# Optimization experiments

Measured on AMD Instinct MI355X. Metric: run time of the kernel, lower is better.

Reference implementation:

```python
import jax, jax.numpy as jnp
import numpy as np

B, S, E, H, D, W = 2, 4096, 768, 12, 64, 256  # batch, seq, hidden, heads, head_dim, one-sided window


def setup_inputs() -> dict:
    key = jax.random.key(0)
    ks = jax.random.split(key, 4)
    s = 0.02
    return {
        "hidden_states": jax.random.normal(ks[0], (B, S, E), jnp.float32),
        "Wq": jax.random.normal(ks[1], (E, E), jnp.float32) * s,
        "bq": jnp.zeros((E,), jnp.float32),
        "Wk": jax.random.normal(ks[2], (E, E), jnp.float32) * s,
        "bk": jnp.zeros((E,), jnp.float32),
        "Wv": jax.random.normal(ks[3], (E, E), jnp.float32) * s,
        "bv": jnp.zeros((E,), jnp.float32),
    }


def _band_attention(q, k, v):
    # q,k,v: [B,H,S,D]. Sliding-window attention: query i attends keys j with |j-i| <= W,
    # clipped to [0, S) -- same math as sliding_chunks_matmul_qk + mask_invalid_locations
    # + softmax + sliding_chunks_matmul_pv (dropout p=0, eval mode).
    C = S // W  # number of query chunks of size W

    def ext(x):
        # gather, for each chunk c, the keys of chunks c-1, c, c+1 (zero padded at edges)
        xp = jnp.pad(x, ((0, 0), (0, 0), (W, W), (0, 0)))
        xc = xp.reshape(B, H, C + 2, W, D)
        return jnp.concatenate([xc[:, :, 0:C], xc[:, :, 1:C + 1], xc[:, :, 2:C + 2]], axis=3)  # [B,H,C,3W,D]

    qc = q.reshape(B, H, C, W, D)
    ke = ext(k)
    ve = ext(v)
    scores = jnp.einsum('bhcpd,bhctd->bhcpt', qc, ke)  # [B,H,C,W,3W]

    p = jnp.arange(W)[:, None]            # query offset within chunk
    t = jnp.arange(3 * W)[None, :]        # key offset within extended window
    rel = t - W - p                       # j - i  (relative position)
    j = jnp.arange(C)[:, None, None] * W + (t - W)[None]  # global key index [C,W,3W]
    mask = (jnp.abs(rel)[None] <= W) & (j >= 0) & (j < S)  # band + sequence-boundary mask

    scores = jnp.where(mask[None, None], scores, -1e30)
    probs = jax.nn.softmax(scores, axis=-1)
    out = jnp.einsum('bhcpt,bhctd->bhcpd', probs, ve)
    return out.reshape(B, H, S, D)


def reference(hidden_states, Wq, bq, Wk, bk, Wv, bv):
    scale = 1.0 / float(np.sqrt(D))
    q = (hidden_states @ Wq + bq) * scale  # q scaled by 1/sqrt(head_dim) as in original
    k = hidden_states @ Wk + bk
    v = hidden_states @ Wv + bv
    split = lambda x: x.reshape(B, S, H, D).transpose(0, 2, 1, 3)  # [B,H,S,D]
    out = _band_attention(split(q), split(k), split(v))
    return out.transpose(0, 2, 1, 3).reshape(B, S, E)  # [B,S,E] context_layer
```

## Files before the change

### kernel.cpp

```cpp
#include <hip/hip_runtime.h>

#define BB 2
#define SS 4096
#define EE 768
#define HH 12
#define DD 64
#define WW 256

typedef __attribute__((ext_vector_type(8))) short short8;
typedef __attribute__((ext_vector_type(4))) short short4v;
typedef __attribute__((ext_vector_type(4))) float floatx4;

#define MFMA16(a, b, c) __builtin_amdgcn_mfma_f32_16x16x32_bf16(a, b, c, 0, 0, 0)

__device__ __forceinline__ float bf2f(short x) {
    union { unsigned u; float f; } v;
    v.u = ((unsigned)(unsigned short)x) << 16;
    return v.f;
}

__device__ __forceinline__ short f2bf(float x) {
    union { float f; unsigned u; } v;
    v.f = x;
    unsigned r = v.u + 0x7fffu + ((v.u >> 16) & 1u);
    return (short)(r >> 16);
}

__device__ __forceinline__ int imin(int a, int b) { return a < b ? a : b; }
__device__ __forceinline__ int imax(int a, int b) { return a > b ? a : b; }

__device__ __forceinline__ void gload_lds16(const short* g, short* l) {
    __builtin_amdgcn_global_load_lds(
        (const __attribute__((address_space(1))) unsigned*)g,
        (__attribute__((address_space(3))) unsigned*)l, 16, 0, 0);
}

__global__ __launch_bounds__(256) void prep(
    const float* __restrict__ hidden, const float* __restrict__ W0,
    const float* __restrict__ W1, const float* __restrict__ W2,
    short* __restrict__ Xb, short* __restrict__ Wt) {
    __shared__ short t[32][33];
    int bid = blockIdx.x;
    int tid = threadIdx.x;
    if (bid < 6144) {
        size_t i4 = (size_t)bid * 256 + tid;
        floatx4 f = *(const floatx4*)(hidden + i4 * 4);
        short4v s;
#pragma unroll
        for (int k = 0; k < 4; k++) s[k] = f2bf(f[k]);
        *(short4v*)(Xb + i4 * 4) = s;
    } else {
        int tmp = bid - 6144;
        int z = tmp / 576, r = tmp % 576;
        int bx = r % 24, by = r / 24;
        const float* in = (z == 0) ? W0 : (z == 1) ? W1 : W2;
        short* op = Wt + (size_t)z * EE * EE;
        int y0 = by * 32;
        int ty = tid >> 3, tx4 = tid & 7;
        floatx4 f = *(const floatx4*)&in[(size_t)(y0 + ty) * EE + bx * 32 + tx4 * 4];
#pragma unroll
        for (int k = 0; k < 4; k++) t[ty][tx4 * 4 + k] = f2bf(f[k]);
        __syncthreads();
        int A = tid >> 3, B0 = (tid & 7) * 4;
        short4v v;
#pragma unroll
        for (int k = 0; k < 4; k++) v[k] = t[B0 + k][A];
        *(short4v*)&op[(size_t)(bx * 32 + A) * EE + y0 + B0] = v;
    }
}

__global__ __launch_bounds__(256, 4) void qkv_gemm(
    const short* __restrict__ Xb, const short* __restrict__ Wt,
    const float* __restrict__ Bq, const float* __restrict__ Bk, const float* __restrict__ Bv,
    short* __restrict__ Qo, short* __restrict__ Ko, short* __restrict__ Vto) {
    int z = blockIdx.z;
    const short* Wz = Wt + (size_t)z * EE * EE;
    const float* bias = (z == 0) ? Bq : (z == 1) ? Bk : Bv;

    __shared__ __align__(16) short As[3][64 * 32];
    __shared__ __align__(16) short Bs[3][128 * 32];
    int tid = threadIdx.x;
    int m0 = blockIdx.x * 64, n0 = blockIdx.y * 128;
    int wave = tid >> 6, lane = tid & 63, lquad = lane >> 4, lrow = lane & 15;
    int wm = (wave & 1) * 32, wn = (wave >> 1) * 64;

    floatx4 acc[2][4] = {};

    int ca = tid;
    int ua = (ca & 7) ^ ((ca >> 3) & 7);
    int ras = (ca >> 3) * 2 + (ua >> 2), qas = (ua & 3) * 8;
    int cb1 = 256 + tid;
    int ub1 = (cb1 & 7) ^ ((cb1 >> 3) & 7);
    int rb1 = (cb1 >> 3) * 2 + (ub1 >> 2), qb1 = (ub1 & 3) * 8;

    const short* xa = &Xb[(size_t)(m0 + ras) * EE + qas];
    const short* wa0 = &Wz[(size_t)(n0 + ras) * EE + qas];
    const short* wa1 = &Wz[(size_t)(n0 + rb1) * EE + qb1];

    auto issueTile = [&](int t) {
        int k0 = t * 32;
        int bs = t % 3;
        gload_lds16(xa + k0, &As[bs][ca * 8]);
        gload_lds16(wa0 + k0, &Bs[bs][ca * 8]);
        gload_lds16(wa1 + k0, &Bs[bs][cb1 * 8]);
    };

    int offA[2], offB[4];
#pragma unroll
    for (int mt = 0; mt < 2; mt++) {
        int ra = wm + mt * 16 + lrow;
        int sa = (lquad | ((ra & 1) << 2)) ^ ((ra >> 1) & 7);
        offA[mt] = (ra >> 1) * 64 + sa * 8;
    }
#pragma unroll
    for (int nt = 0; nt < 4; nt++) {
        int rb = wn + nt * 16 + lrow;
        int sb = (lquad | ((rb & 1) << 2)) ^ ((rb >> 1) & 7);
        offB[nt] = (rb >> 1) * 64 + sb * 8;
    }

    issueTile(0);
    issueTile(1);

#pragma unroll
    for (int t = 0; t < 24; ++t) {
        if (t < 23) asm volatile("s_waitcnt vmcnt(3)" ::: "memory");
        else        asm volatile("s_waitcnt vmcnt(0)" ::: "memory");
        __builtin_amdgcn_sched_barrier(0);
        __builtin_amdgcn_s_barrier();
        asm volatile("" ::: "memory");

        if (t + 2 < 24) issueTile(t + 2);

        int bs = t % 3;
        short8 af[2], bfv[4];
#pragma unroll
        for (int mt = 0; mt < 2; mt++)
            af[mt] = *(short8*)&As[bs][offA[mt]];
#pragma unroll
        for (int nt = 0; nt < 4; nt++)
            bfv[nt] = *(short8*)&Bs[bs][offB[nt]];
#pragma unroll
        for (int mt = 0; mt < 2; mt++)
#pragma unroll
            for (int nt = 0; nt < 4; nt++)
                acc[mt][nt] = MFMA16(af[mt], bfv[nt], acc[mt][nt]);
    }

    if (z == 2) {
        for (int nt = 0; nt < 4; nt++) {
            int gn = n0 + wn + nt * 16 + lrow;
            float bv = bias[gn];
            int h = gn >> 6, d = gn & 63;
            for (int mt = 0; mt < 2; mt++) {
                int gm0 = m0 + wm + mt * 16 + lquad * 4;
                int b = gm0 >> 12, s = gm0 & (SS - 1);
                short4v pk;
                for (int r = 0; r < 4; r++) pk[r] = f2bf(acc[mt][nt][r] + bv);
                *(short4v*)&Vto[(((size_t)(b * HH + h)) * DD + d) * SS + s] = pk;
            }
        }
    } else {
        short* out = (z == 0) ? Qo : Ko;
        float scale = (z == 0) ? 0.125f : 1.0f;
        for (int nt = 0; nt < 4; nt++) {
            int gn = n0 + wn + nt * 16 + lrow;
            float bv = bias[gn];
            int h = gn >> 6, d = gn & 63;
            for (int mt = 0; mt < 2; mt++) {
                int gmb = m0 + wm + mt * 16 + lquad * 4;
                for (int r = 0; r < 4; r++) {
                    int gm = gmb + r;
                    int b = gm >> 12, s = gm & (SS - 1);
                    float v = (acc[mt][nt][r] + bv) * scale;
                    out[(((size_t)(b * HH + h)) * SS + s) * DD + d] = f2bf(v);
                }
            }
        }
    }
}

__global__ __launch_bounds__(256) void band_attn(
    const short* __restrict__ Q, const short* __restrict__ K,
    const short* __restrict__ Vt, float* __restrict__ out) {
    int hb = blockIdx.x;
    int h = hb % HH, b = hb / HH;
    int chunk = blockIdx.y;
    int tid = threadIdx.x;
    int wave = tid >> 6, lane = tid & 63, lquad = lane >> 4, lrow = lane & 15;
    int qbase = chunk * 128 + wave * 32;

    const short* Qh = Q + ((size_t)(b * HH + h)) * SS * DD;
    const short* Kh = K + ((size_t)(b * HH + h)) * SS * DD;
    const short* Vh = Vt + ((size_t)(b * HH + h)) * DD * SS;

    __shared__ __align__(16) short Ks[2][64 * 72];
    __shared__ __align__(16) short Vs[2][64 * 72];
    __shared__ __align__(16) short Ps[4][16 * 72];
    short* Pw = &Ps[wave][0];

    short8 qf[2][2];
#pragma unroll
    for (int m = 0; m < 2; m++)
#pragma unroll
        for (int hh = 0; hh < 2; hh++)
            qf[m][hh] = *(const short8*)&Qh[(size_t)(qbase + m * 16 + lrow) * DD + hh * 32 + lquad * 8];

    floatx4 o[2][4] = {};
    float ls[2] = {0.0f, 0.0f};

    int kwin = chunk * 128 - WW;
    int srow = tid >> 3;
    int scol = (tid & 7) * 8;
    int tlo = wave >> 1;

    short8 kreg[2], vreg[2];
    auto loadTile = [&](int t) {
        int ks0 = kwin + t * 64;
#pragma unroll
        for (int i = 0; i < 2; i++) {
            int r = srow + i * 32;
            int gk = imin(imax(ks0 + r, 0), SS - 1);
            kreg[i] = *(const short8*)&Kh[(size_t)gk * DD + scol];
            int gv = imin(imax(ks0 + scol, 0), SS - 8);
            vreg[i] = *(const short8*)&Vh[(size_t)r * SS + gv];
        }
    };
    auto storeTile = [&](int buf) {
#pragma unroll
        for (int i = 0; i < 2; i++) {
            int r = srow + i * 32;
            *(short8*)&Ks[buf][r * 72 + scol] = kreg[i];
            *(short8*)&Vs[buf][r * 72 + scol] = vreg[i];
        }
    };

    loadTile(0);
    storeTile(0);
    __syncthreads();

    for (int t = 0; t < 10; t++) {
        int buf = t & 1;
        if (t < 9) loadTile(t + 1);

        if ((unsigned)(t - tlo) < 9u) {
            int ks0 = kwin + t * 64;
            short8 kf[4][2], vf[4][2];
#pragma unroll
            for (int kt = 0; kt < 4; kt++)
#pragma unroll
                for (int hh = 0; hh < 2; hh++)
                    kf[kt][hh] = *(short8*)&Ks[buf][(kt * 16 + lrow) * 72 + hh * 32 + lquad * 8];
#pragma unroll
            for (int nt = 0; nt < 4; nt++)
#pragma unroll
                for (int hh = 0; hh < 2; hh++)
                    vf[nt][hh] = *(short8*)&Vs[buf][(nt * 16 + lrow) * 72 + hh * 32 + lquad * 8];

            int d0 = ks0 - qbase;
            bool interior = (d0 >= -225) && (d0 <= 193) && (ks0 >= 0) && (ks0 <= SS - 64);

            __builtin_amdgcn_s_setprio(1);
#pragma unroll
            for (int m = 0; m < 2; m++) {
                int q = qbase + m * 16 + lrow;
                floatx4 s[4];
#pragma unroll
                for (int kt = 0; kt < 4; kt++) {
                    floatx4 zz = {};
                    s[kt] = MFMA16(kf[kt][0], qf[m][0], zz);
                    s[kt] = MFMA16(kf[kt][1], qf[m][1], s[kt]);
                }
                float lacc = 0.0f;
                if (interior) {
#pragma unroll
                    for (int kt = 0; kt < 4; kt++) {
                        short4v pk;
#pragma unroll
                        for (int r = 0; r < 4; r++) {
                            float p = __expf(s[kt][r]);
                            pk[r] = f2bf(p);
                            lacc += bf2f(pk[r]);
                        }
                        *(short4v*)&Pw[lrow * 72 + kt * 16 + lquad * 4] = pk;
                    }
                } else {
#pragma unroll
                    for (int kt = 0; kt < 4; kt++) {
                        short4v pk;
#pragma unroll
                        for (int r = 0; r < 4; r++) {
                            int key = ks0 + kt * 16 + lquad * 4 + r;
                            bool valid = ((unsigned)(key - q + WW) <= 2u * WW) && ((unsigned)key < SS);
                            float p = valid ? __expf(s[kt][r]) : 0.0f;
                            pk[r] = f2bf(p);
                            lacc += bf2f(pk[r]);
                        }
                        *(short4v*)&Pw[lrow * 72 + kt * 16 + lquad * 4] = pk;
                    }
                }
                ls[m] += lacc;
                asm volatile("" ::: "memory");
                short8 ap0 = *(short8*)&Pw[lrow * 72 + lquad * 8];
                short8 ap1 = *(short8*)&Pw[lrow * 72 + 32 + lquad * 8];
#pragma unroll
                for (int nt = 0; nt < 4; nt++) {
                    o[m][nt] = MFMA16(ap0, vf[nt][0], o[m][nt]);
                    o[m][nt] = MFMA16(ap1, vf[nt][1], o[m][nt]);
                }
            }
            __builtin_amdgcn_s_setprio(0);
        }

        if (t < 9) storeTile(buf ^ 1);
        __syncthreads();
    }

#pragma unroll
    for (int m = 0; m < 2; m++) {
        ls[m] += __shfl_xor(ls[m], 16, 64);
        ls[m] += __shfl_xor(ls[m], 32, 64);
        ls[m] = 1.0f / ls[m];
    }

#pragma unroll
    for (int m = 0; m < 2; m++) {
#pragma unroll
        for (int r = 0; r < 4; r++) {
            float linv = __shfl(ls[m], lquad * 4 + r, 64);
            int s = qbase + m * 16 + lquad * 4 + r;
#pragma unroll
            for (int nt = 0; nt < 4; nt++)
                out[((size_t)b * SS + s) * EE + h * DD + nt * 16 + lrow] = o[m][nt][r] * linv;
        }
    }
}

extern "C" void kernel_launch(void* const* d_in, const int* in_sizes, int n_in,
                              void* d_out, int out_size, void* d_ws, size_t ws_size,
                              hipStream_t stream) {
    const float* hidden = (const float*)d_in[0];
    const float* Wq = (const float*)d_in[1];
    const float* bq = (const float*)d_in[2];
    const float* Wk = (const float*)d_in[3];
    const float* bk = (const float*)d_in[4];
    const float* Wv = (const float*)d_in[5];
    const float* bv = (const float*)d_in[6];
    float* out = (float*)d_out;

    short* ws = (short*)d_ws;
    const size_t WSZ = (size_t)EE * EE;
    const size_t QSZ = (size_t)BB * HH * SS * DD;
    short* Wt = ws;
    short* Qb = Wt + 3 * WSZ;
    short* Kb = Qb + QSZ;
    short* Vtb = Kb + QSZ;
    short* Xb = (short*)d_out;

    prep<<<dim3(6144 + 3 * 576, 1, 1), 256, 0, stream>>>(hidden, Wq, Wk, Wv, Xb, Wt);

    qkv_gemm<<<dim3(128, 6, 3), 256, 0, stream>>>(Xb, Wt, bq, bk, bv, Qb, Kb, Vtb);

    band_attn<<<dim3(HH * BB, SS / 128, 1), 256, 0, stream>>>(Qb, Kb, Vtb, out);
}
```

Baseline: 184.5 us.

## Fuse fp32-to-bf16 conversion of hidden states into the QKV GEMM A-tile load

The separate prep pass that converted hidden states to bf16 is removed. The GEMM now loads fp32 activations into registers, converts them, and writes them to LDS, double-buffered across iterations, while B tiles still stream directly into LDS. This saves a full write and re-read of the bf16 activation copy. In exchange it reads twice the bytes for A, and every z-slice and n-block converts the same rows again. It also adds register pressure and an extra LDS wait and barrier per iteration.

```diff
diff --git a/kernel.cpp b/kernel.cpp
--- a/kernel.cpp
+++ b/kernel.cpp
@@ -36,41 +36,30 @@
 }
 
 __global__ __launch_bounds__(256) void prep(
-    const float* __restrict__ hidden, const float* __restrict__ W0,
-    const float* __restrict__ W1, const float* __restrict__ W2,
-    short* __restrict__ Xb, short* __restrict__ Wt) {
+    const float* __restrict__ W0, const float* __restrict__ W1,
+    const float* __restrict__ W2, short* __restrict__ Wt) {
     __shared__ short t[32][33];
     int bid = blockIdx.x;
     int tid = threadIdx.x;
-    if (bid < 6144) {
-        size_t i4 = (size_t)bid * 256 + tid;
-        floatx4 f = *(const floatx4*)(hidden + i4 * 4);
-        short4v s;
-#pragma unroll
-        for (int k = 0; k < 4; k++) s[k] = f2bf(f[k]);
-        *(short4v*)(Xb + i4 * 4) = s;
-    } else {
-        int tmp = bid - 6144;
-        int z = tmp / 576, r = tmp % 576;
-        int bx = r % 24, by = r / 24;
-        const float* in = (z == 0) ? W0 : (z == 1) ? W1 : W2;
-        short* op = Wt + (size_t)z * EE * EE;
-        int y0 = by * 32;
-        int ty = tid >> 3, tx4 = tid & 7;
-        floatx4 f = *(const floatx4*)&in[(size_t)(y0 + ty) * EE + bx * 32 + tx4 * 4];
-#pragma unroll
-        for (int k = 0; k < 4; k++) t[ty][tx4 * 4 + k] = f2bf(f[k]);
-        __syncthreads();
-        int A = tid >> 3, B0 = (tid & 7) * 4;
-        short4v v;
-#pragma unroll
-        for (int k = 0; k < 4; k++) v[k] = t[B0 + k][A];
-        *(short4v*)&op[(size_t)(bx * 32 + A) * EE + y0 + B0] = v;
-    }
+    int z = bid / 576, r = bid % 576;
+    int bx = r % 24, by = r / 24;
+    const float* in = (z == 0) ? W0 : (z == 1) ? W1 : W2;
+    short* op = Wt + (size_t)z * EE * EE;
+    int y0 = by * 32;
+    int ty = tid >> 3, tx4 = tid & 7;
+    floatx4 f = *(const floatx4*)&in[(size_t)(y0 + ty) * EE + bx * 32 + tx4 * 4];
+#pragma unroll
+    for (int k = 0; k < 4; k++) t[ty][tx4 * 4 + k] = f2bf(f[k]);
+    __syncthreads();
+    int A = tid >> 3, B0 = (tid & 7) * 4;
+    short4v v;
+#pragma unroll
+    for (int k = 0; k < 4; k++) v[k] = t[B0 + k][A];
+    *(short4v*)&op[(size_t)(bx * 32 + A) * EE + y0 + B0] = v;
 }
 
 __global__ __launch_bounds__(256, 4) void qkv_gemm(
-    const short* __restrict__ Xb, const short* __restrict__ Wt,
+    const float* __restrict__ X, const short* __restrict__ Wt,
     const float* __restrict__ Bq, const float* __restrict__ Bk, const float* __restrict__ Bv,
     short* __restrict__ Qo, short* __restrict__ Ko, short* __restrict__ Vto) {
     int z = blockIdx.z;
@@ -92,25 +81,30 @@
     int cb1 = 256 + tid;
     int ub1 = (cb1 & 7) ^ ((cb1 >> 3) & 7);
     int rb1 = (cb1 >> 3) * 2 + (ub1 >> 2), qb1 = (ub1 & 3) * 8;
-
-    const short* xa = &Xb[(size_t)(m0 + ras) * EE + qas];
     const short* wa0 = &Wz[(size_t)(n0 + ras) * EE + qas];
     const short* wa1 = &Wz[(size_t)(n0 + rb1) * EE + qb1];
 
-    auto issueTile = [&](int t) {
-        int k0 = t * 32;
-        int bs = t % 3;
-        gload_lds16(xa + k0, &As[bs][ca * 8]);
+    int ra = tid >> 2, qa = tid & 3;
+    int cA = (ra >> 1) * 8 + ((qa | ((ra & 1) << 2)) ^ ((ra >> 1) & 7));
+    const float* xsrc = &X[(size_t)(m0 + ra) * EE + qa * 8];
+
+    auto issueB = [&](int t) {
+        int k0 = t * 32, bs = t % 3;
         gload_lds16(wa0 + k0, &Bs[bs][ca * 8]);
         gload_lds16(wa1 + k0, &Bs[bs][cb1 * 8]);
     };
 
+#define ISSUE_A(r0, r1, t) { const floatx4* p = (const floatx4*)(xsrc + (t) * 32); r0 = p[0]; r1 = p[1]; }
+#define WRITE_A(r0, r1, t) { short8 s8_; \
+    _Pragma("unroll") for (int j_ = 0; j_ < 4; j_++) { s8_[j_] = f2bf(r0[j_]); s8_[j_ + 4] = f2bf(r1[j_]); } \
+    *(short8*)&As[(t) % 3][cA * 8] = s8_; }
+
     int offA[2], offB[4];
 #pragma unroll
     for (int mt = 0; mt < 2; mt++) {
-        int ra = wm + mt * 16 + lrow;
-        int sa = (lquad | ((ra & 1) << 2)) ^ ((ra >> 1) & 7);
-        offA[mt] = (ra >> 1) * 64 + sa * 8;
+        int rr = wm + mt * 16 + lrow;
+        int sa = (lquad | ((rr & 1) << 2)) ^ ((rr >> 1) & 7);
+        offA[mt] = (rr >> 1) * 64 + sa * 8;
     }
 #pragma unroll
     for (int nt = 0; nt < 4; nt++) {
@@ -119,32 +113,47 @@
         offB[nt] = (rb >> 1) * 64 + sb * 8;
     }
 
-    issueTile(0);
-    issueTile(1);
+    floatx4 a0A, a1A, a0B, a1B;
+
+    issueB(0); ISSUE_A(a0A, a1A, 0);
+    issueB(1); ISSUE_A(a0B, a1B, 1);
+    asm volatile("s_waitcnt vmcnt(4)" ::: "memory");
+    WRITE_A(a0A, a1A, 0);
+    asm volatile("s_waitcnt lgkmcnt(0)" ::: "memory");
+    __builtin_amdgcn_s_barrier();
+    asm volatile("" ::: "memory");
 
 #pragma unroll
     for (int t = 0; t < 24; ++t) {
-        if (t < 23) asm volatile("s_waitcnt vmcnt(3)" ::: "memory");
-        else        asm volatile("s_waitcnt vmcnt(0)" ::: "memory");
+        if (t + 2 < 24) {
+            issueB(t + 2);
+            if (t & 1) { ISSUE_A(a0B, a1B, t + 2); } else { ISSUE_A(a0A, a1A, t + 2); }
+        }
+
+        int bs = t % 3;
+        short8 af[2], bfv[4];
+#pragma unroll
+        for (int mt = 0; mt < 2; mt++)
+            af[mt] = *(short8*)&As[bs][offA[mt]];
+#pragma unroll
+        for (int nt = 0; nt < 4; nt++)
+            bfv[nt] = *(short8*)&Bs[bs][offB[nt]];
+#pragma unroll
+        for (int mt = 0; mt < 2; mt++)
+#pragma unroll
+            for (int nt = 0; nt < 4; nt++)
+                acc[mt][nt] = MFMA16(af[mt], bfv[nt], acc[mt][nt]);
+
+        if (t + 1 < 24) {
+            if (t + 2 < 24) asm volatile("s_waitcnt vmcnt(4)" ::: "memory");
+            else            asm volatile("s_waitcnt vmcnt(0)" ::: "memory");
+            if (t & 1) { WRITE_A(a0A, a1A, t + 1); } else { WRITE_A(a0B, a1B, t + 1); }
+        }
+
         __builtin_amdgcn_sched_barrier(0);
+        asm volatile("s_waitcnt lgkmcnt(0)" ::: "memory");
         __builtin_amdgcn_s_barrier();
         asm volatile("" ::: "memory");
-
-        if (t + 2 < 24) issueTile(t + 2);
-
-        int bs = t % 3;
-        short8 af[2], bfv[4];
-#pragma unroll
-        for (int mt = 0; mt < 2; mt++)
-            af[mt] = *(short8*)&As[bs][offA[mt]];
-#pragma unroll
-        for (int nt = 0; nt < 4; nt++)
-            bfv[nt] = *(short8*)&Bs[bs][offB[nt]];
-#pragma unroll
-        for (int mt = 0; mt < 2; mt++)
-#pragma unroll
-            for (int nt = 0; nt < 4; nt++)
-                acc[mt][nt] = MFMA16(af[mt], bfv[nt], acc[mt][nt]);
     }
 
     if (z == 2) {
@@ -178,6 +187,8 @@
             }
         }
     }
+#undef ISSUE_A
+#undef WRITE_A
 }
 
 __global__ __launch_bounds__(256) void band_attn(
@@ -355,11 +366,10 @@
     short* Qb = Wt + 3 * WSZ;
     short* Kb = Qb + QSZ;
     short* Vtb = Kb + QSZ;
-    short* Xb = (short*)d_out;
-
-    prep<<<dim3(6144 + 3 * 576, 1, 1), 256, 0, stream>>>(hidden, Wq, Wk, Wv, Xb, Wt);
-
-    qkv_gemm<<<dim3(128, 6, 3), 256, 0, stream>>>(Xb, Wt, bq, bk, bv, Qb, Kb, Vtb);
+
+    prep<<<dim3(3 * 576, 1, 1), 256, 0, stream>>>(Wq, Wk, Wv, Wt);
+
+    qkv_gemm<<<dim3(128, 6, 3), 256, 0, stream>>>(hidden, Wt, bq, bk, bv, Qb, Kb, Vtb);
 
     band_attn<<<dim3(HH * BB, SS / 128, 1), 256, 0, stream>>>(Qb, Kb, Vtb, out);
 }
```

After: 182.4 us. No clear change (-1.1%).

## Replace LDS-staged pipelined QKV GEMM with direct global-to-register fragment loads

Applied to the files above, without the earlier changes.

The QKV projection GEMM drops its triple-buffered LDS staging (global_load_lds with swizzled layout, waitcnt and barriers). Each wave now loads its MFMA A and B fragments straight from global memory into registers inside a fully unrolled k-loop. The aim is to remove LDS traffic, barriers and the occupancy limit set by shared memory, relying on L1/L2 caching for reuse. In exchange, operand reuse across waves is lost and global load traffic rises, with no explicit prefetch pipeline, so the loop may stall on memory latency. The launch-bounds occupancy hint is also removed.

```diff
diff --git a/kernel.cpp b/kernel.cpp
--- a/kernel.cpp
+++ b/kernel.cpp
@@ -28,12 +28,6 @@
 
 __device__ __forceinline__ int imin(int a, int b) { return a < b ? a : b; }
 __device__ __forceinline__ int imax(int a, int b) { return a > b ? a : b; }
-
-__device__ __forceinline__ void gload_lds16(const short* g, short* l) {
-    __builtin_amdgcn_global_load_lds(
-        (const __attribute__((address_space(1))) unsigned*)g,
-        (__attribute__((address_space(3))) unsigned*)l, 16, 0, 0);
-}
 
 __global__ __launch_bounds__(256) void prep(
     const float* __restrict__ hidden, const float* __restrict__ W0,
@@ -69,7 +63,7 @@
     }
 }
 
-__global__ __launch_bounds__(256, 4) void qkv_gemm(
+__global__ __launch_bounds__(256) void qkv_gemm(
     const short* __restrict__ Xb, const short* __restrict__ Wt,
     const float* __restrict__ Bq, const float* __restrict__ Bk, const float* __restrict__ Bv,
     short* __restrict__ Qo, short* __restrict__ Ko, short* __restrict__ Vto) {
@@ -77,8 +71,6 @@
     const short* Wz = Wt + (size_t)z * EE * EE;
     const float* bias = (z == 0) ? Bq : (z == 1) ? Bk : Bv;
 
-    __shared__ __align__(16) short As[3][64 * 32];
-    __shared__ __align__(16) short Bs[3][128 * 32];
     int tid = threadIdx.x;
     int m0 = blockIdx.x * 64, n0 = blockIdx.y * 128;
     int wave = tid >> 6, lane = tid & 63, lquad = lane >> 4, lrow = lane & 15;
@@ -86,65 +78,30 @@
 
     floatx4 acc[2][4] = {};
 
-    int ca = tid;
-    int ua = (ca & 7) ^ ((ca >> 3) & 7);
-    int ras = (ca >> 3) * 2 + (ua >> 2), qas = (ua & 3) * 8;
-    int cb1 = 256 + tid;
-    int ub1 = (cb1 & 7) ^ ((cb1 >> 3) & 7);
-    int rb1 = (cb1 >> 3) * 2 + (ub1 >> 2), qb1 = (ub1 & 3) * 8;
-
-    const short* xa = &Xb[(size_t)(m0 + ras) * EE + qas];
-    const short* wa0 = &Wz[(size_t)(n0 + ras) * EE + qas];
-    const short* wa1 = &Wz[(size_t)(n0 + rb1) * EE + qb1];
-
-    auto issueTile = [&](int t) {
+    const short* abase0 = &Xb[(size_t)(m0 + wm + 0 * 16 + lrow) * EE + lquad * 8];
+    const short* abase1 = &Xb[(size_t)(m0 + wm + 1 * 16 + lrow) * EE + lquad * 8];
+    const short* bbase0 = &Wz[(size_t)(n0 + wn + 0 * 16 + lrow) * EE + lquad * 8];
+    const short* bbase1 = &Wz[(size_t)(n0 + wn + 1 * 16 + lrow) * EE + lquad * 8];
+    const short* bbase2 = &Wz[(size_t)(n0 + wn + 2 * 16 + lrow) * EE + lquad * 8];
+    const short* bbase3 = &Wz[(size_t)(n0 + wn + 3 * 16 + lrow) * EE + lquad * 8];
+
+#pragma unroll
+    for (int t = 0; t < 24; ++t) {
         int k0 = t * 32;
-        int bs = t % 3;
-        gload_lds16(xa + k0, &As[bs][ca * 8]);
-        gload_lds16(wa0 + k0, &Bs[bs][ca * 8]);
-        gload_lds16(wa1 + k0, &Bs[bs][cb1 * 8]);
-    };
-
-    int offA[2], offB[4];
-#pragma unroll
-    for (int mt = 0; mt < 2; mt++) {
-        int ra = wm + mt * 16 + lrow;
-        int sa = (lquad | ((ra & 1) << 2)) ^ ((ra >> 1) & 7);
-        offA[mt] = (ra >> 1) * 64 + sa * 8;
-    }
-#pragma unroll
-    for (int nt = 0; nt < 4; nt++) {
-        int rb = wn + nt * 16 + lrow;
-        int sb = (lquad | ((rb & 1) << 2)) ^ ((rb >> 1) & 7);
-        offB[nt] = (rb >> 1) * 64 + sb * 8;
-    }
-
-    issueTile(0);
-    issueTile(1);
-
-#pragma unroll
-    for (int t = 0; t < 24; ++t) {
-        if (t < 23) asm volatile("s_waitcnt vmcnt(3)" ::: "memory");
-        else        asm volatile("s_waitcnt vmcnt(0)" ::: "memory");
-        __builtin_amdgcn_sched_barrier(0);
-        __builtin_amdgcn_s_barrier();
-        asm volatile("" ::: "memory");
-
-        if (t + 2 < 24) issueTile(t + 2);
-
-        int bs = t % 3;
-        short8 af[2], bfv[4];
-#pragma unroll
-        for (int mt = 0; mt < 2; mt++)
-            af[mt] = *(short8*)&As[bs][offA[mt]];
-#pragma unroll
-        for (int nt = 0; nt < 4; nt++)
-            bfv[nt] = *(short8*)&Bs[bs][offB[nt]];
-#pragma unroll
-        for (int mt = 0; mt < 2; mt++)
-#pragma unroll
-            for (int nt = 0; nt < 4; nt++)
-                acc[mt][nt] = MFMA16(af[mt], bfv[nt], acc[mt][nt]);
+        short8 af0 = *(const short8*)(abase0 + k0);
+        short8 af1 = *(const short8*)(abase1 + k0);
+        short8 bf0 = *(const short8*)(bbase0 + k0);
+        short8 bf1 = *(const short8*)(bbase1 + k0);
+        short8 bf2 = *(const short8*)(bbase2 + k0);
+        short8 bf3 = *(const short8*)(bbase3 + k0);
+        acc[0][0] = MFMA16(af0, bf0, acc[0][0]);
+        acc[0][1] = MFMA16(af0, bf1, acc[0][1]);
+        acc[0][2] = MFMA16(af0, bf2, acc[0][2]);
+        acc[0][3] = MFMA16(af0, bf3, acc[0][3]);
+        acc[1][0] = MFMA16(af1, bf0, acc[1][0]);
+        acc[1][1] = MFMA16(af1, bf1, acc[1][1]);
+        acc[1][2] = MFMA16(af1, bf2, acc[1][2]);
+        acc[1][3] = MFMA16(af1, bf3, acc[1][3]);
     }
 
     if (z == 2) {
```

Result: slower. 274.3 us (+48.7%).
